# Kernel optimization log

Hardware: AMD Instinct MI355X
Metric: run time of the kernel (lower is better)

Reference implementation:

```python
import jax, jax.numpy as jnp
import numpy as np

BIG = 1e9  # self-distance masking constant, as in the torch module


def setup_inputs() -> dict:
    key = jax.random.key(0)
    k1, _ = jax.random.split(key)
    coords = jax.random.normal(k1, (8, 4096, 3), dtype=jnp.float32)
    mask = jnp.ones((8, 4096), dtype=bool)
    return {"coords": coords, "mask": mask}


def reference(coords, mask):
    # coords: [B, N, 3]; mask is accepted but unused (matches the torch module)
    B, N, _ = coords.shape
    # Pairwise Euclidean distances via the |a|^2 + |b|^2 - 2ab identity
    # (avoids materializing the [B,N,N,3] diff tensor the torch code builds).
    sq = jnp.sum(coords * coords, axis=-1)                      # [B, N]
    inner = jnp.einsum('bnd,bmd->bnm', coords, coords)          # [B, N, N]
    d2 = sq[:, :, None] + sq[:, None, :] - 2.0 * inner
    dist = jnp.sqrt(jnp.maximum(d2, 0.0))                       # [B, N, N]
    dist = dist + jnp.eye(N, dtype=dist.dtype) * BIG            # mask self
    # argsort(dim=2)[:, :, :2] == indices of the two smallest distances
    _, idx = jax.lax.top_k(-dist, 2)                            # [B, N, 2]
    first_nearest_indices = idx[:, :, 0]
    second_nearest_indices = idx[:, :, 1]
    A = jnp.take_along_axis(
        coords, jnp.broadcast_to(first_nearest_indices[:, :, None], (B, N, 3)), axis=1)
    C = jnp.take_along_axis(
        coords, jnp.broadcast_to(second_nearest_indices[:, :, None], (B, N, 3)), axis=1)
    return (A, C, first_nearest_indices, second_nearest_indices)
```

## Files before the change

### kernel.cpp

```cpp
#include <hip/hip_runtime.h>

#define BATCH 8
#define NPTS 4096
#define TOTQ (BATCH * NPTS)
#define TPB 256
#define NCH 64
#define CSZ 64
#define QF 8
#define QPB 16
#define BIGD 1e30f
#define MAXI 0x7fffffff

__device__ __forceinline__ float cand_w(float x, float y, float z) {
    return fmaf(x, x, fmaf(y, y, z * z));
}
__device__ __forceinline__ float cand_key(float cx, float cy, float cz, float w,
                                          float xn, float yn, float zn) {
    return fmaf(cx, xn, fmaf(cy, yn, fmaf(cz, zn, w)));
}

__device__ __forceinline__ void lexup(float k, int i,
                                      float& b1, int& i1,
                                      float& b2, int& i2) {
    bool c1 = (k < b1) || (k == b1 && i < i1);
    bool c2 = (k < b2) || (k == b2 && i < i2);
    float nb2 = c1 ? b1 : (c2 ? k : b2);
    int   ni2 = c1 ? i1 : (c2 ? i : i2);
    b1 = c1 ? k : b1;
    i1 = c1 ? i : i1;
    b2 = nb2;
    i2 = ni2;
}

__global__ __launch_bounds__(TPB) void knn_scan_v(const float* __restrict__ coords,
                                                  float2* __restrict__ vals) {
    __shared__ float4 pts[CSZ];
    const int tid   = (int)threadIdx.x;
    const int tile  = blockIdx.x;
    const int chunk = blockIdx.y;
    const int b     = blockIdx.z;
    const float* basep = coords + (size_t)b * NPTS * 3;
    const int mbase = chunk * CSZ;

    if (tid < CSZ) {
        float x = basep[(mbase + tid) * 3 + 0];
        float y = basep[(mbase + tid) * 3 + 1];
        float z = basep[(mbase + tid) * 3 + 2];
        pts[tid] = make_float4(-2.0f * x, -2.0f * y, -2.0f * z, cand_w(x, y, z));
    }

    const int qbase = tile * (TPB * QF);
    float xn[QF], yn[QF], zn[QF], b1[QF], b2[QF];
#pragma unroll
    for (int q = 0; q < QF; ++q) {
        int n = qbase + q * TPB + tid;
        xn[q] = basep[n * 3 + 0];
        yn[q] = basep[n * 3 + 1];
        zn[q] = basep[n * 3 + 2];
        b1[q] = BIGD; b2[q] = BIGD;
    }
    __syncthreads();

    for (int p = 0; p < CSZ; p += 4) {
        float4 c[4];
#pragma unroll
        for (int j = 0; j < 4; ++j) c[j] = pts[p + j];
#pragma unroll
        for (int j = 0; j < 4; ++j) {
#pragma unroll
            for (int q = 0; q < QF; ++q) {
                float k = cand_key(c[j].x, c[j].y, c[j].z, c[j].w, xn[q], yn[q], zn[q]);
                b2[q] = fminf(fmaxf(k, b1[q]), b2[q]);
                b1[q] = fminf(k, b1[q]);
            }
        }
    }

#pragma unroll
    for (int q = 0; q < QF; ++q) {
        int n = qbase + q * TPB + tid;
        vals[(size_t)chunk * TOTQ + (size_t)b * NPTS + n] = make_float2(b1[q], b2[q]);
    }
}

__global__ __launch_bounds__(TPB) void knn_merge_w(const float* __restrict__ coords,
                                                   const float2* __restrict__ vals,
                                                   float* __restrict__ out) {
    __shared__ float4 part[16][QPB];
    __shared__ int4 rl[QPB];
    __shared__ int2 res[QPB];
    const int t  = (int)threadIdx.x;
    const int qb = blockIdx.x * QPB;
    const int b  = qb >> 12;
    const int c_self = (qb & (NPTS - 1)) >> 6;
    const float* bp = coords + (size_t)b * NPTS * 3;

    {
        const int s  = t >> 4;
        const int qi = t & 15;
        const int q  = qb + qi;
        float f1 = BIGD, f2 = BIGD;
        int t1 = MAXI, t2 = MAXI;
#pragma unroll
        for (int u = 0; u < 4; ++u) {
            const int c = s * 4 + u;
            if (c == c_self) continue;
            float2 v = vals[(size_t)c * TOTQ + q];
            lexup(v.x, 2 * c + 0, f1, t1, f2, t2);
            lexup(v.y, 2 * c + 1, f1, t1, f2, t2);
        }
        part[s][qi] = make_float4(f1, __int_as_float(t1), f2, __int_as_float(t2));
    }
    __syncthreads();

    if (t < QPB) {
        float f1 = BIGD, f2 = BIGD;
        int t1 = MAXI, t2 = MAXI;
#pragma unroll
        for (int ss = 0; ss < 16; ++ss) {
            float4 p = part[ss][t];
            lexup(p.x, __float_as_int(p.y), f1, t1, f2, t2);
            lexup(p.z, __float_as_int(p.w), f1, t1, f2, t2);
        }
        const int ca = t1 >> 1;
        const int cb = t2 >> 1;
        const int lo = min(min(ca, cb), c_self);
        const int hi = max(max(ca, cb), c_self);
        const int md = ca + cb + c_self - lo - hi;
        rl[t] = make_int4(lo, md, hi, 0);
    }
    __syncthreads();

    {
        const int lane = t & 63;
        const int w = t >> 6;
        for (int j = 0; j < 4; ++j) {
            const int qj = w * 4 + j;
            const int4 r = rl[qj];
            const int n = (qb + qj) & (NPTS - 1);
            const float xq = bp[n * 3 + 0];
            const float yq = bp[n * 3 + 1];
            const float zq = bp[n * 3 + 2];

            const int m0 = r.x * CSZ + lane;
            const int m1 = r.y * CSZ + lane;
            const int m2 = r.z * CSZ + lane;
            float cx0 = bp[m0 * 3 + 0], cy0 = bp[m0 * 3 + 1], cz0 = bp[m0 * 3 + 2];
            float cx1 = bp[m1 * 3 + 0], cy1 = bp[m1 * 3 + 1], cz1 = bp[m1 * 3 + 2];
            float cx2 = bp[m2 * 3 + 0], cy2 = bp[m2 * 3 + 1], cz2 = bp[m2 * 3 + 2];

            float b1 = BIGD, b2 = BIGD;
            int i1 = MAXI, i2 = MAXI;
            {
                float k = cand_key(-2.0f * cx0, -2.0f * cy0, -2.0f * cz0,
                                   cand_w(cx0, cy0, cz0), xq, yq, zq);
                const bool self = (m0 == n);
                lexup(self ? BIGD : k, self ? MAXI : m0, b1, i1, b2, i2);
            }
            if (r.y != r.x) {
                float k = cand_key(-2.0f * cx1, -2.0f * cy1, -2.0f * cz1,
                                   cand_w(cx1, cy1, cz1), xq, yq, zq);
                const bool self = (m1 == n);
                lexup(self ? BIGD : k, self ? MAXI : m1, b1, i1, b2, i2);
            }
            if (r.z != r.y) {
                float k = cand_key(-2.0f * cx2, -2.0f * cy2, -2.0f * cz2,
                                   cand_w(cx2, cy2, cz2), xq, yq, zq);
                const bool self = (m2 == n);
                lexup(self ? BIGD : k, self ? MAXI : m2, b1, i1, b2, i2);
            }
#pragma unroll
            for (int off = 1; off < 64; off <<= 1) {
                const float ok1 = __shfl_xor(b1, off);
                const int   oi1 = __shfl_xor(i1, off);
                const float ok2 = __shfl_xor(b2, off);
                const int   oi2 = __shfl_xor(i2, off);
                lexup(ok1, oi1, b1, i1, b2, i2);
                lexup(ok2, oi2, b1, i1, b2, i2);
            }
            if (lane == 0) res[qj] = make_int2(i1, i2);
        }
    }
    __syncthreads();

    if (t < 48) {
        const int qj = t / 3;
        const int d  = t % 3;
        const int q  = qb + qj;
        const int i1 = res[qj].x;
        const int i2 = res[qj].y;
        float* A = out;
        float* C = out + (size_t)TOTQ * 3;
        A[(size_t)q * 3 + d] = bp[i1 * 3 + d];
        C[(size_t)q * 3 + d] = bp[i2 * 3 + d];
    }
    if (t < QPB) {
        const int q = qb + t;
        float* I1 = out + (size_t)2 * TOTQ * 3;
        float* I2 = I1 + (size_t)TOTQ;
        I1[q] = (float)res[t].x;
        I2[q] = (float)res[t].y;
    }
}

__device__ __forceinline__ void top2min(float k, int m,
                                        float& b1, int& i1,
                                        float& b2, int& i2) {
    bool c1 = k < b1;
    bool c2 = k < b2;
    int ni2 = c2 ? m : i2;
    i2 = c1 ? i1 : ni2;
    i1 = c1 ? m : i1;
    b2 = fminf(fmaxf(k, b1), b2);
    b1 = fminf(k, b1);
}

__global__ __launch_bounds__(TPB) void knn_full(const float* __restrict__ coords,
                                                float* __restrict__ out) {
    __shared__ float4 pts[NPTS];
    const int tid  = (int)threadIdx.x;
    const int tile = blockIdx.x;
    const int b    = blockIdx.y;
    const float* basep = coords + (size_t)b * NPTS * 3;

    for (int p = tid; p < NPTS; p += TPB) {
        float x = basep[p * 3 + 0];
        float y = basep[p * 3 + 1];
        float z = basep[p * 3 + 2];
        pts[p] = make_float4(-2.0f * x, -2.0f * y, -2.0f * z, cand_w(x, y, z));
    }
    const int n = tile * TPB + tid;
    const float xn = basep[n * 3 + 0];
    const float yn = basep[n * 3 + 1];
    const float zn = basep[n * 3 + 2];
    __syncthreads();

    float b1 = BIGD, b2 = BIGD;
    int i1 = 0, i2 = 0;
    for (int p = 0; p < NPTS; p += 4) {
#pragma unroll
        for (int j = 0; j < 4; ++j) {
            float4 c = pts[p + j];
            float k = cand_key(c.x, c.y, c.z, c.w, xn, yn, zn);
            k = (p + j == n) ? BIGD : k;
            top2min(k, p + j, b1, i1, b2, i2);
        }
    }

    const int q = b * NPTS + n;
    float* A  = out;
    float* C  = out + (size_t)TOTQ * 3;
    float* I1 = out + (size_t)2 * TOTQ * 3;
    float* I2 = I1 + (size_t)TOTQ;
    float4 p1 = pts[i1];
    float4 p2 = pts[i2];
    A[(size_t)q * 3 + 0] = -0.5f * p1.x;
    A[(size_t)q * 3 + 1] = -0.5f * p1.y;
    A[(size_t)q * 3 + 2] = -0.5f * p1.z;
    C[(size_t)q * 3 + 0] = -0.5f * p2.x;
    C[(size_t)q * 3 + 1] = -0.5f * p2.y;
    C[(size_t)q * 3 + 2] = -0.5f * p2.z;
    I1[q] = (float)i1;
    I2[q] = (float)i2;
}

extern "C" void kernel_launch(void* const* d_in, const int* in_sizes, int n_in,
                              void* d_out, int out_size, void* d_ws, size_t ws_size,
                              hipStream_t stream) {
    const float* coords = (const float*)d_in[0];
    float* out = (float*)d_out;

    const size_t need = (size_t)NCH * TOTQ * sizeof(float2);
    if (ws_size >= need) {
        float2* vals = (float2*)d_ws;
        hipLaunchKernelGGL(knn_scan_v, dim3(NPTS / (TPB * QF), NCH, BATCH), dim3(TPB),
                           0, stream, coords, vals);
        hipLaunchKernelGGL(knn_merge_w, dim3(TOTQ / QPB), dim3(TPB), 0, stream,
                           coords, vals, out);
    } else {
        hipLaunchKernelGGL(knn_full, dim3(NPTS / TPB, BATCH), dim3(TPB), 0, stream,
                           coords, out);
    }
}
```

Measured before the change: 99.76 us.

## Fuse scan and merge into one cooperative kernel with grid sync

Replaces the two-launch scan/merge pipeline with a single cooperative kernel of 512 blocks. Each block runs two scan units, waits at a grid-wide barrier, then runs two merge units. Merge blocks now handle 32 queries instead of 16, halving the merge block count. The aim is to cut the second launch and the tail/drain cost between kernels, in exchange for grid-sync overhead and lower parallelism per phase. If the cooperative launch fails, it falls back to the two-kernel path.

```diff
diff --git a/kernel.cpp b/kernel.cpp
--- a/kernel.cpp
+++ b/kernel.cpp
@@ -1,4 +1,7 @@
 #include <hip/hip_runtime.h>
+#include <hip/hip_cooperative_groups.h>
+
+namespace cg = cooperative_groups;
 
 #define BATCH 8
 #define NPTS 4096
@@ -7,7 +10,8 @@
 #define NCH 64
 #define CSZ 64
 #define QF 8
-#define QPB 16
+#define QPB 32
+#define CGRID 512
 #define BIGD 1e30f
 #define MAXI 0x7fffffff
 
@@ -32,28 +36,28 @@
     i2 = ni2;
 }
 
-__global__ __launch_bounds__(TPB) void knn_scan_v(const float* __restrict__ coords,
-                                                  float2* __restrict__ vals) {
-    __shared__ float4 pts[CSZ];
-    const int tid   = (int)threadIdx.x;
-    const int tile  = blockIdx.x;
-    const int chunk = blockIdx.y;
-    const int b     = blockIdx.z;
+__device__ __forceinline__ void scan_unit(int sbx, int t,
+                                          const float* __restrict__ coords,
+                                          float2* __restrict__ vals,
+                                          float4* pts) {
+    const int tile  = sbx & 1;
+    const int chunk = (sbx >> 1) & 63;
+    const int b     = sbx >> 7;
     const float* basep = coords + (size_t)b * NPTS * 3;
     const int mbase = chunk * CSZ;
 
-    if (tid < CSZ) {
-        float x = basep[(mbase + tid) * 3 + 0];
-        float y = basep[(mbase + tid) * 3 + 1];
-        float z = basep[(mbase + tid) * 3 + 2];
-        pts[tid] = make_float4(-2.0f * x, -2.0f * y, -2.0f * z, cand_w(x, y, z));
+    if (t < CSZ) {
+        float x = basep[(mbase + t) * 3 + 0];
+        float y = basep[(mbase + t) * 3 + 1];
+        float z = basep[(mbase + t) * 3 + 2];
+        pts[t] = make_float4(-2.0f * x, -2.0f * y, -2.0f * z, cand_w(x, y, z));
     }
 
     const int qbase = tile * (TPB * QF);
     float xn[QF], yn[QF], zn[QF], b1[QF], b2[QF];
 #pragma unroll
     for (int q = 0; q < QF; ++q) {
-        int n = qbase + q * TPB + tid;
+        int n = qbase + q * TPB + t;
         xn[q] = basep[n * 3 + 0];
         yn[q] = basep[n * 3 + 1];
         zn[q] = basep[n * 3 + 2];
@@ -78,32 +82,31 @@
 
 #pragma unroll
     for (int q = 0; q < QF; ++q) {
-        int n = qbase + q * TPB + tid;
+        int n = qbase + q * TPB + t;
         vals[(size_t)chunk * TOTQ + (size_t)b * NPTS + n] = make_float2(b1[q], b2[q]);
     }
-}
-
-__global__ __launch_bounds__(TPB) void knn_merge_w(const float* __restrict__ coords,
-                                                   const float2* __restrict__ vals,
-                                                   float* __restrict__ out) {
-    __shared__ float4 part[16][QPB];
-    __shared__ int4 rl[QPB];
-    __shared__ int2 res[QPB];
-    const int t  = (int)threadIdx.x;
-    const int qb = blockIdx.x * QPB;
+    __syncthreads();
+}
+
+__device__ __forceinline__ void merge_unit(int mbx, int t,
+                                           const float* __restrict__ coords,
+                                           const float2* __restrict__ vals,
+                                           float* __restrict__ out,
+                                           float4 (*part)[QPB], int4* rl, int2* res) {
+    const int qb = mbx * QPB;
     const int b  = qb >> 12;
     const int c_self = (qb & (NPTS - 1)) >> 6;
     const float* bp = coords + (size_t)b * NPTS * 3;
 
     {
-        const int s  = t >> 4;
-        const int qi = t & 15;
+        const int s  = t >> 5;
+        const int qi = t & 31;
         const int q  = qb + qi;
         float f1 = BIGD, f2 = BIGD;
         int t1 = MAXI, t2 = MAXI;
 #pragma unroll
-        for (int u = 0; u < 4; ++u) {
-            const int c = s * 4 + u;
+        for (int u = 0; u < 8; ++u) {
+            const int c = s * 8 + u;
             if (c == c_self) continue;
             float2 v = vals[(size_t)c * TOTQ + q];
             lexup(v.x, 2 * c + 0, f1, t1, f2, t2);
@@ -117,7 +120,7 @@
         float f1 = BIGD, f2 = BIGD;
         int t1 = MAXI, t2 = MAXI;
 #pragma unroll
-        for (int ss = 0; ss < 16; ++ss) {
+        for (int ss = 0; ss < 8; ++ss) {
             float4 p = part[ss][t];
             lexup(p.x, __float_as_int(p.y), f1, t1, f2, t2);
             lexup(p.z, __float_as_int(p.w), f1, t1, f2, t2);
@@ -134,8 +137,8 @@
     {
         const int lane = t & 63;
         const int w = t >> 6;
-        for (int j = 0; j < 4; ++j) {
-            const int qj = w * 4 + j;
+        for (int j = 0; j < 8; ++j) {
+            const int qj = w * 8 + j;
             const int4 r = rl[qj];
             const int n = (qb + qj) & (NPTS - 1);
             const float xq = bp[n * 3 + 0];
@@ -183,16 +186,14 @@
     }
     __syncthreads();
 
-    if (t < 48) {
+    if (t < 96) {
         const int qj = t / 3;
         const int d  = t % 3;
         const int q  = qb + qj;
-        const int i1 = res[qj].x;
-        const int i2 = res[qj].y;
         float* A = out;
         float* C = out + (size_t)TOTQ * 3;
-        A[(size_t)q * 3 + d] = bp[i1 * 3 + d];
-        C[(size_t)q * 3 + d] = bp[i2 * 3 + d];
+        A[(size_t)q * 3 + d] = bp[res[qj].x * 3 + d];
+        C[(size_t)q * 3 + d] = bp[res[qj].y * 3 + d];
     }
     if (t < QPB) {
         const int q = qb + t;
@@ -201,6 +202,42 @@
         I1[q] = (float)res[t].x;
         I2[q] = (float)res[t].y;
     }
+    __syncthreads();
+}
+
+__global__ __launch_bounds__(TPB) void knn_fused(const float* __restrict__ coords,
+                                                 float2* __restrict__ vals,
+                                                 float* __restrict__ out) {
+    __shared__ float4 pts[CSZ];
+    __shared__ float4 part[8][QPB];
+    __shared__ int4 rl[QPB];
+    __shared__ int2 res[QPB];
+    const int t  = (int)threadIdx.x;
+    const int bx = (int)blockIdx.x;
+
+    scan_unit(bx,         t, coords, vals, pts);
+    scan_unit(bx + CGRID, t, coords, vals, pts);
+
+    cg::this_grid().sync();
+
+    merge_unit(bx,         t, coords, vals, out, part, rl, res);
+    merge_unit(bx + CGRID, t, coords, vals, out, part, rl, res);
+}
+
+__global__ __launch_bounds__(TPB) void knn_scan_v(const float* __restrict__ coords,
+                                                  float2* __restrict__ vals) {
+    __shared__ float4 pts[CSZ];
+    const int bx = (int)blockIdx.x;
+    scan_unit(bx, (int)threadIdx.x, coords, vals, pts);
+}
+
+__global__ __launch_bounds__(TPB) void knn_merge_w(const float* __restrict__ coords,
+                                                   const float2* __restrict__ vals,
+                                                   float* __restrict__ out) {
+    __shared__ float4 part[8][QPB];
+    __shared__ int4 rl[QPB];
+    __shared__ int2 res[QPB];
+    merge_unit((int)blockIdx.x, (int)threadIdx.x, coords, vals, out, part, rl, res);
 }
 
 __device__ __forceinline__ void top2min(float k, int m,
@@ -273,10 +310,16 @@
     const size_t need = (size_t)NCH * TOTQ * sizeof(float2);
     if (ws_size >= need) {
         float2* vals = (float2*)d_ws;
-        hipLaunchKernelGGL(knn_scan_v, dim3(NPTS / (TPB * QF), NCH, BATCH), dim3(TPB),
-                           0, stream, coords, vals);
-        hipLaunchKernelGGL(knn_merge_w, dim3(TOTQ / QPB), dim3(TPB), 0, stream,
-                           coords, vals, out);
+        void* args[] = { (void*)&coords, (void*)&vals, (void*)&out };
+        hipError_t err = hipLaunchCooperativeKernel((const void*)knn_fused,
+                                                    dim3(CGRID), dim3(TPB),
+                                                    args, 0, stream);
+        if (err != hipSuccess) {
+            hipLaunchKernelGGL(knn_scan_v, dim3(1024), dim3(TPB), 0, stream,
+                               coords, vals);
+            hipLaunchKernelGGL(knn_merge_w, dim3(TOTQ / QPB), dim3(TPB), 0, stream,
+                               coords, vals, out);
+        }
     } else {
         hipLaunchKernelGGL(knn_full, dim3(NPTS / TPB, BATCH), dim3(TPB), 0, stream,
                            coords, out);
```

Result: slower. 172.8 us (+73.2%).
